# Performance work log

Hardware: AMD Instinct MI355X
Metric: run time of the kernel (lower is better)

The kernel has to match this reference:

```python
import jax, jax.numpy as jnp
import numpy as np

B, S, D, H = 2, 2048, 1024, 16
HD = D // H  # 64

def setup_inputs() -> dict:
    key = jax.random.key(0)
    k1, k2, k3 = jax.random.split(key, 3)
    x = jax.random.normal(k1, (B, S, D), dtype=jnp.float32)
    w_qkv = jax.random.normal(k2, (D, 3 * D), dtype=jnp.float32) * 0.02
    w_out = jax.random.normal(k3, (D, D), dtype=jnp.float32) * 0.02
    b_out = jnp.zeros((D,), dtype=jnp.float32)
    return {"x": x, "w_qkv": w_qkv, "w_out": w_out, "b_out": b_out}

def reference(x, w_qkv, w_out, b_out):
    # fused qkv projection (no bias)
    qkv = jnp.einsum('bsd,de->bse', x, w_qkv)            # [B,S,3D]
    q, k, v = jnp.split(qkv, 3, axis=-1)                 # each [B,S,D]
    def split_heads(t):
        return t.reshape(B, S, H, HD).transpose(0, 2, 1, 3)  # [B,H,S,HD]
    q, k, v = split_heads(q), split_heads(k), split_heads(v)
    scores = jnp.einsum('bhqd,bhkd->bhqk', q, k) / jnp.sqrt(jnp.float32(HD))
    probs = jax.nn.softmax(scores, axis=-1)              # [B,H,S,S]
    attn = jnp.einsum('bhqk,bhkd->bhqd', probs, v)       # [B,H,S,HD]
    attn = attn.transpose(0, 2, 1, 3).reshape(B, S, D)   # [B,S,D]
    out = jnp.einsum('bsd,de->bse', attn, w_out) + b_out
    return out
```

## Files before the change

### kernel.cpp

```cpp
#include <hip/hip_runtime.h>
#include <stdint.h>

#define B_  2
#define S_  2048
#define D_  1024
#define H_  16
#define HD_ 64
#define KVT 128
#define NT  (S_ / KVT)

typedef __attribute__((ext_vector_type(8))) short short8;
typedef __attribute__((ext_vector_type(4))) float f32x4;

__device__ inline unsigned short f2bf(float f) {
  union { float f; unsigned int i; } u; u.f = f;
  unsigned int r = u.i + 0x7FFFu + ((u.i >> 16) & 1u);
  return (unsigned short)(r >> 16);
}

__device__ inline uint32_t cvtpk_bf16(float lo, float hi) {
  uint32_t r;
  asm("v_cvt_pk_bf16_f32 %0, %1, %2" : "=v"(r) : "v"(lo), "v"(hi));
  return r;
}

__device__ inline float fexp2(float x) {
  float r;
  asm("v_exp_f32 %0, %1" : "=v"(r) : "v"(x));
  return r;
}

__device__ inline void gload16(const void* g, void* l) {
  __builtin_amdgcn_global_load_lds(
      (const __attribute__((address_space(1))) void*)g,
      (__attribute__((address_space(3))) void*)l,
      16, 0, 0);
}

__global__ __launch_bounds__(256)
void prologue_kernel(const float* __restrict__ x, unsigned short* __restrict__ xb,
                     const float* __restrict__ w_qkv, unsigned short* __restrict__ wqkvT,
                     const float* __restrict__ w_out, unsigned short* __restrict__ woutT) {
  __shared__ float tile[32][33];
  const int bid = blockIdx.x;
  const int t = threadIdx.x;

  if (bid < 4096) {
    int i = (bid * 256 + t) * 4;
    float4 v = *(const float4*)(x + i);
    union { unsigned short s[4]; uint2 v; } o;
    o.s[0] = f2bf(v.x); o.s[1] = f2bf(v.y); o.s[2] = f2bf(v.z); o.s[3] = f2bf(v.w);
    *(uint2*)(xb + i) = o.v;
    return;
  }

  const float* in;
  unsigned short* out;
  int R, C, bx, by;
  if (bid < 4096 + 3072) {
    int tid = bid - 4096;
    in = w_qkv; out = wqkvT; R = 1024; C = 3072;
    bx = tid % 96; by = tid / 96;
  } else {
    int tid = bid - 7168;
    in = w_out; out = woutT; R = 1024; C = 1024;
    bx = tid & 31; by = tid >> 5;
  }
  const int tx = t & 31, ty = t >> 5;
#pragma unroll
  for (int i = 0; i < 4; ++i)
    tile[ty + i * 8][tx] = in[(size_t)(by * 32 + ty + i * 8) * C + bx * 32 + tx];
  __syncthreads();
#pragma unroll
  for (int i = 0; i < 4; ++i)
    out[(size_t)(bx * 32 + ty + i * 8) * R + by * 32 + tx] = f2bf(tile[tx][ty + i * 8]);
}

__global__ __launch_bounds__(256, 3)
void gemm_qkv(const unsigned short* __restrict__ A,
              const unsigned short* __restrict__ Bt,
              unsigned short* __restrict__ qw,
              unsigned short* __restrict__ kw,
              unsigned short* __restrict__ vTw) {
  const int K = 1024;
  __shared__ __align__(16) unsigned short As[128 * 64];
  __shared__ __align__(16) unsigned short Bs[128 * 64];
  const int t  = threadIdx.x;
  const int w  = t >> 6, l = t & 63;
  const int lr = l & 15, lg = l >> 4;
  const int wr = w >> 1, wc = w & 1;
  const int bn = blockIdx.x, bm = blockIdx.y;

  const int srow = t >> 3;
  const int scol = 8 * ((t & 7) ^ (srow & 7));

  const unsigned short* Ab = A  + (size_t)(bm * 128 + srow) * K + scol;
  const unsigned short* Bb = Bt + (size_t)(bn * 128 + srow) * K + scol;

  f32x4 acc[4][4];
#pragma unroll
  for (int m = 0; m < 4; ++m)
#pragma unroll
    for (int n = 0; n < 4; ++n)
      acc[m][n] = (f32x4){0.f, 0.f, 0.f, 0.f};

  for (int kt = 0; kt < K; kt += 64) {
#pragma unroll
    for (int i = 0; i < 4; ++i) {
      gload16(Ab + (size_t)i * 32 * K + kt, &As[(size_t)(i * 256 + t) * 8]);
      gload16(Bb + (size_t)i * 32 * K + kt, &Bs[(size_t)(i * 256 + t) * 8]);
    }
    __syncthreads();
#pragma unroll
    for (int ks = 0; ks < 2; ++ks) {
      short8 af[4], bf[4];
#pragma unroll
      for (int m = 0; m < 4; ++m) {
        int row = wr * 64 + m * 16 + lr;
        af[m] = *(const short8*)&As[row * 64 + ((ks * 32 + lg * 8) ^ ((row & 7) * 8))];
      }
#pragma unroll
      for (int n = 0; n < 4; ++n) {
        int row = wc * 64 + n * 16 + lr;
        bf[n] = *(const short8*)&Bs[row * 64 + ((ks * 32 + lg * 8) ^ ((row & 7) * 8))];
      }
#pragma unroll
      for (int m = 0; m < 4; ++m)
#pragma unroll
        for (int n = 0; n < 4; ++n)
          acc[m][n] = __builtin_amdgcn_mfma_f32_16x16x32_bf16(af[m], bf[n], acc[m][n], 0, 0, 0);
    }
    __syncthreads();
  }

#pragma unroll
  for (int m = 0; m < 4; ++m)
#pragma unroll
    for (int n = 0; n < 4; ++n)
#pragma unroll
      for (int r = 0; r < 4; ++r) {
        float v = acc[m][n][r];
        int i = bm * 128 + wr * 64 + m * 16 + lg * 4 + r;
        int j = bn * 128 + wc * 64 + n * 16 + lr;
        int b = i >> 11, s = i & 2047;
        int part = j >> 10, rem = j & 1023, h = rem >> 6, hd = rem & 63;
        size_t bh = (size_t)(b * H_ + h);
        if (part == 0) {
          qw[(bh * S_ + s) * HD_ + hd] = f2bf(v * 0.1803368801f);
        } else if (part == 1) {
          kw[(bh * S_ + s) * HD_ + hd] = f2bf(v);
        } else {
          int s6 = s & 63;
          int sp = (s & ~63) | (s6 & 32) | (((s6 >> 2) & 3) << 3)
                 | (((s6 >> 4) & 1) << 2) | (s6 & 3);
          vTw[(bh * HD_ + hd) * S_ + sp] = f2bf(v);
        }
      }
}

__global__ __launch_bounds__(256)
void gemm_out(const unsigned short* __restrict__ A,
              const unsigned short* __restrict__ Bt,
              float* __restrict__ out,
              const float* __restrict__ bias) {
  const int K = 1024;
  __shared__ __align__(16) unsigned short As[128 * 64];
  __shared__ __align__(16) unsigned short Bs[64 * 64];
  const int t  = threadIdx.x;
  const int w  = t >> 6, l = t & 63;
  const int lr = l & 15, lg = l >> 4;
  const int wr = w >> 1, wc = w & 1;
  const int bn = blockIdx.x, bm = blockIdx.y;

  const int srow = t >> 3;
  const int scol = 8 * ((t & 7) ^ (srow & 7));

  const unsigned short* Ab = A  + (size_t)(bm * 128 + srow) * K + scol;
  const unsigned short* Bb = Bt + (size_t)(bn * 64 + srow) * K + scol;

  f32x4 acc[4][2];
#pragma unroll
  for (int m = 0; m < 4; ++m)
#pragma unroll
    for (int n = 0; n < 2; ++n)
      acc[m][n] = (f32x4){0.f, 0.f, 0.f, 0.f};

  for (int kt = 0; kt < K; kt += 64) {
#pragma unroll
    for (int i = 0; i < 4; ++i)
      gload16(Ab + (size_t)i * 32 * K + kt, &As[(size_t)(i * 256 + t) * 8]);
#pragma unroll
    for (int i = 0; i < 2; ++i)
      gload16(Bb + (size_t)i * 32 * K + kt, &Bs[(size_t)(i * 256 + t) * 8]);
    __syncthreads();
#pragma unroll
    for (int ks = 0; ks < 2; ++ks) {
      short8 af[4], bf[2];
#pragma unroll
      for (int m = 0; m < 4; ++m) {
        int row = wr * 64 + m * 16 + lr;
        af[m] = *(const short8*)&As[row * 64 + ((ks * 32 + lg * 8) ^ ((row & 7) * 8))];
      }
#pragma unroll
      for (int n = 0; n < 2; ++n) {
        int row = wc * 32 + n * 16 + lr;
        bf[n] = *(const short8*)&Bs[row * 64 + ((ks * 32 + lg * 8) ^ ((row & 7) * 8))];
      }
#pragma unroll
      for (int m = 0; m < 4; ++m)
#pragma unroll
        for (int n = 0; n < 2; ++n)
          acc[m][n] = __builtin_amdgcn_mfma_f32_16x16x32_bf16(af[m], bf[n], acc[m][n], 0, 0, 0);
    }
    __syncthreads();
  }

#pragma unroll
  for (int m = 0; m < 4; ++m)
#pragma unroll
    for (int n = 0; n < 2; ++n)
#pragma unroll
      for (int r = 0; r < 4; ++r) {
        int i = bm * 128 + wr * 64 + m * 16 + lg * 4 + r;
        int j = bn * 64 + wc * 32 + n * 16 + lr;
        out[(size_t)i * D_ + j] = acc[m][n][r] + bias[j];
      }
}

__global__ __launch_bounds__(256, 2)
void attn_kernel(const unsigned short* __restrict__ qw,
                 const unsigned short* __restrict__ kw,
                 const unsigned short* __restrict__ vTw,
                 unsigned short* __restrict__ attn) {
  __shared__ __align__(16) unsigned short Ks[2][KVT * 64];
  __shared__ __align__(16) unsigned short Vs[2][64 * KVT];

  const int t  = threadIdx.x;
  const int w  = t >> 6, l = t & 63;
  const int lr = l & 15, lg = l >> 4;

  const int bid = blockIdx.x;
  const int bh = (bid & 7) * 4 + ((bid >> 3) & 3);
  const int qt = bid >> 5;

  const int q0 = qt * 128 + w * 32;
  const unsigned short* Qb = qw  + (size_t)bh * S_ * HD_;
  const unsigned short* Kb = kw  + (size_t)bh * S_ * HD_;
  const unsigned short* Vb = vTw + (size_t)bh * HD_ * S_;

  const int krow = t >> 3, kcol = 8 * ((t & 7) ^ ((t >> 3) & 7));
  const int vrow = t >> 4, vcol = 8 * ((t & 15) ^ ((t >> 4) & 7));

  const short8 ones = {16256, 16256, 16256, 16256, 16256, 16256, 16256, 16256};
  const f32x4 FZERO = (f32x4){0.f, 0.f, 0.f, 0.f};

  short8 qf[2][2];
#pragma unroll
  for (int m = 0; m < 2; ++m)
#pragma unroll
    for (int ks = 0; ks < 2; ++ks)
      qf[m][ks] = *(const short8*)&Qb[(size_t)(q0 + m * 16 + lr) * HD_ + ks * 32 + lg * 8];

  f32x4 of[2][4];
  f32x4 osum[2];
#pragma unroll
  for (int m = 0; m < 2; ++m) {
#pragma unroll
    for (int n = 0; n < 4; ++n) of[m][n] = FZERO;
    osum[m] = FZERO;
  }

#pragma unroll
  for (int i = 0; i < 4; ++i) {
    gload16(Kb + (size_t)(i * 32 + krow) * HD_ + kcol, &Ks[0][(i * 256 + t) * 8]);
    gload16(Vb + (size_t)(i * 16 + vrow) * S_ + vcol,  &Vs[0][(i * 256 + t) * 8]);
  }
  __syncthreads();

  int cur = 0;
  for (int tt = 0; tt < NT; ++tt) {
    if (tt + 1 < NT) {
      const int kt = (tt + 1) * KVT;
#pragma unroll
      for (int i = 0; i < 4; ++i) {
        gload16(Kb + (size_t)(kt + i * 32 + krow) * HD_ + kcol, &Ks[cur ^ 1][(i * 256 + t) * 8]);
        gload16(Vb + (size_t)(i * 16 + vrow) * S_ + kt + vcol,  &Vs[cur ^ 1][(i * 256 + t) * 8]);
      }
    }

    f32x4 sfT[2][8];
    __builtin_amdgcn_s_setprio(1);
#pragma unroll
    for (int n = 0; n < 8; ++n) {
      int row = n * 16 + lr;
      short8 kf0 = *(const short8*)&Ks[cur][row * 64 + ((lg * 8) ^ ((row & 7) * 8))];
      sfT[0][n] = __builtin_amdgcn_mfma_f32_16x16x32_bf16(kf0, qf[0][0], FZERO, 0, 0, 0);
      sfT[1][n] = __builtin_amdgcn_mfma_f32_16x16x32_bf16(kf0, qf[1][0], FZERO, 0, 0, 0);
      short8 kf1 = *(const short8*)&Ks[cur][row * 64 + ((32 + lg * 8) ^ ((row & 7) * 8))];
      sfT[0][n] = __builtin_amdgcn_mfma_f32_16x16x32_bf16(kf1, qf[0][1], sfT[0][n], 0, 0, 0);
      sfT[1][n] = __builtin_amdgcn_mfma_f32_16x16x32_bf16(kf1, qf[1][1], sfT[1][n], 0, 0, 0);
    }
    __builtin_amdgcn_s_setprio(0);

    union { uint32_t u[4]; short8 v; } pb[2][4];
#pragma unroll
    for (int m = 0; m < 2; ++m) {
#pragma unroll
      for (int n = 0; n < 8; ++n) {
        sfT[m][n][0] = fexp2(sfT[m][n][0]);
        sfT[m][n][1] = fexp2(sfT[m][n][1]);
        sfT[m][n][2] = fexp2(sfT[m][n][2]);
        sfT[m][n][3] = fexp2(sfT[m][n][3]);
      }
#pragma unroll
      for (int kk = 0; kk < 4; ++kk) {
        pb[m][kk].u[0] = cvtpk_bf16(sfT[m][2 * kk][0],     sfT[m][2 * kk][1]);
        pb[m][kk].u[1] = cvtpk_bf16(sfT[m][2 * kk][2],     sfT[m][2 * kk][3]);
        pb[m][kk].u[2] = cvtpk_bf16(sfT[m][2 * kk + 1][0], sfT[m][2 * kk + 1][1]);
        pb[m][kk].u[3] = cvtpk_bf16(sfT[m][2 * kk + 1][2], sfT[m][2 * kk + 1][3]);
      }
    }

    __builtin_amdgcn_s_setprio(1);
#pragma unroll
    for (int nd = 0; nd < 4; ++nd)
#pragma unroll
      for (int kk = 0; kk < 4; ++kk) {
        int row = nd * 16 + lr;
        short8 vf = *(const short8*)&Vs[cur][row * 128 + ((kk * 32 + lg * 8) ^ ((row & 7) * 8))];
        of[0][nd] = __builtin_amdgcn_mfma_f32_16x16x32_bf16(vf, pb[0][kk].v, of[0][nd], 0, 0, 0);
        of[1][nd] = __builtin_amdgcn_mfma_f32_16x16x32_bf16(vf, pb[1][kk].v, of[1][nd], 0, 0, 0);
      }
#pragma unroll
    for (int m = 0; m < 2; ++m)
#pragma unroll
      for (int kk = 0; kk < 4; ++kk)
        osum[m] = __builtin_amdgcn_mfma_f32_16x16x32_bf16(ones, pb[m][kk].v, osum[m], 0, 0, 0);
    __builtin_amdgcn_s_setprio(0);

    __syncthreads();
    cur ^= 1;
  }

  const int b = bh >> 4, h = bh & 15;
#pragma unroll
  for (int m = 0; m < 2; ++m) {
    float inv = 1.0f / osum[m][0];
    int q = q0 + m * 16 + lr;
#pragma unroll
    for (int nd = 0; nd < 4; ++nd)
#pragma unroll
      for (int r = 0; r < 4; ++r)
        attn[((size_t)b * S_ + q) * D_ + h * 64 + nd * 16 + lg * 4 + r] =
            f2bf(of[m][nd][r] * inv);
  }
}

extern "C" void kernel_launch(void* const* d_in, const int* in_sizes, int n_in,
                              void* d_out, int out_size, void* d_ws, size_t ws_size,
                              hipStream_t stream) {
  const float* x     = (const float*)d_in[0];
  const float* w_qkv = (const float*)d_in[1];
  const float* w_out = (const float*)d_in[2];
  const float* b_out = (const float*)d_in[3];
  float* out = (float*)d_out;

  char* p = (char*)d_ws;
  unsigned short* xb    = (unsigned short*)p; p += (size_t)4096 * 1024 * 2;
  unsigned short* wqkvT = (unsigned short*)p; p += (size_t)3072 * 1024 * 2;
  unsigned short* woutT = (unsigned short*)p; p += (size_t)1024 * 1024 * 2;
  unsigned short* qws   = (unsigned short*)p; p += (size_t)B_ * H_ * S_ * HD_ * 2;
  unsigned short* kws   = (unsigned short*)p; p += (size_t)B_ * H_ * S_ * HD_ * 2;
  unsigned short* vTws  = (unsigned short*)p; p += (size_t)B_ * H_ * S_ * HD_ * 2;
  unsigned short* attnb = (unsigned short*)p; p += (size_t)4096 * 1024 * 2;

  prologue_kernel<<<8192, 256, 0, stream>>>(x, xb, w_qkv, wqkvT, w_out, woutT);

  gemm_qkv<<<dim3(24, 32), 256, 0, stream>>>(xb, wqkvT, qws, kws, vTws);

  attn_kernel<<<512, 256, 0, stream>>>(qws, kws, vTws, attnb);

  gemm_out<<<dim3(16, 32), 256, 0, stream>>>(attnb, woutT, out, b_out);
}
```

Measured before the change: 102.6 us.

## Split attention KV range in two with partial outputs and a combine kernel

Splits each attention block's KV sequence into two halves, so twice as many blocks run (1024 instead of 512), each over 1024 keys with a 64-wide KV tile and a higher occupancy hint. Each half writes unnormalized bf16 partial outputs and row sums to workspace. A new combine kernel adds the halves, normalizes, and writes the head-interleaved attention output. This aims to fill the CUs better, at the cost of an extra launch, extra global traffic, and an added bf16 rounding of the partials.

```diff
diff --git a/kernel.cpp b/kernel.cpp
--- a/kernel.cpp
+++ b/kernel.cpp
@@ -6,8 +6,8 @@
 #define D_  1024
 #define H_  16
 #define HD_ 64
-#define KVT 128
-#define NT  (S_ / KVT)
+#define KVT 64
+#define NTT 16
 
 typedef __attribute__((ext_vector_type(8))) short short8;
 typedef __attribute__((ext_vector_type(4))) float f32x4;
@@ -16,6 +16,10 @@
   union { float f; unsigned int i; } u; u.f = f;
   unsigned int r = u.i + 0x7FFFu + ((u.i >> 16) & 1u);
   return (unsigned short)(r >> 16);
+}
+
+__device__ inline float bf2f(unsigned short u) {
+  union { unsigned int i; float f; } x; x.i = ((unsigned int)u) << 16; return x.f;
 }
 
 __device__ inline uint32_t cvtpk_bf16(float lo, float hi) {
@@ -227,11 +231,12 @@
       }
 }
 
-__global__ __launch_bounds__(256, 2)
+__global__ __launch_bounds__(256, 4)
 void attn_kernel(const unsigned short* __restrict__ qw,
                  const unsigned short* __restrict__ kw,
                  const unsigned short* __restrict__ vTw,
-                 unsigned short* __restrict__ attn) {
+                 unsigned short* __restrict__ part,
+                 float* __restrict__ sums) {
   __shared__ __align__(16) unsigned short Ks[2][KVT * 64];
   __shared__ __align__(16) unsigned short Vs[2][64 * KVT];
 
@@ -240,16 +245,17 @@
   const int lr = l & 15, lg = l >> 4;
 
   const int bid = blockIdx.x;
-  const int bh = (bid & 7) * 4 + ((bid >> 3) & 3);
-  const int qt = bid >> 5;
+  const int bh   = (bid & 7) * 4 + ((bid >> 3) & 3);
+  const int rest = bid >> 5;
+  const int qt   = rest >> 1;
+  const int half = rest & 1;
 
   const int q0 = qt * 128 + w * 32;
   const unsigned short* Qb = qw  + (size_t)bh * S_ * HD_;
-  const unsigned short* Kb = kw  + (size_t)bh * S_ * HD_;
-  const unsigned short* Vb = vTw + (size_t)bh * HD_ * S_;
+  const unsigned short* Kb = kw  + (size_t)bh * S_ * HD_ + (size_t)half * 1024 * HD_;
+  const unsigned short* Vb = vTw + (size_t)bh * HD_ * S_ + half * 1024;
 
   const int krow = t >> 3, kcol = 8 * ((t & 7) ^ ((t >> 3) & 7));
-  const int vrow = t >> 4, vcol = 8 * ((t & 15) ^ ((t >> 4) & 7));
 
   const short8 ones = {16256, 16256, 16256, 16256, 16256, 16256, 16256, 16256};
   const f32x4 FZERO = (f32x4){0.f, 0.f, 0.f, 0.f};
@@ -271,27 +277,29 @@
   }
 
 #pragma unroll
-  for (int i = 0; i < 4; ++i) {
-    gload16(Kb + (size_t)(i * 32 + krow) * HD_ + kcol, &Ks[0][(i * 256 + t) * 8]);
-    gload16(Vb + (size_t)(i * 16 + vrow) * S_ + vcol,  &Vs[0][(i * 256 + t) * 8]);
+  for (int i = 0; i < 2; ++i) {
+    int row = i * 32 + krow;
+    gload16(Kb + (size_t)row * HD_ + kcol, &Ks[0][(i * 256 + t) * 8]);
+    gload16(Vb + (size_t)row * S_ + kcol,  &Vs[0][(i * 256 + t) * 8]);
   }
   __syncthreads();
 
   int cur = 0;
-  for (int tt = 0; tt < NT; ++tt) {
-    if (tt + 1 < NT) {
+  for (int tt = 0; tt < NTT; ++tt) {
+    if (tt + 1 < NTT) {
       const int kt = (tt + 1) * KVT;
 #pragma unroll
-      for (int i = 0; i < 4; ++i) {
-        gload16(Kb + (size_t)(kt + i * 32 + krow) * HD_ + kcol, &Ks[cur ^ 1][(i * 256 + t) * 8]);
-        gload16(Vb + (size_t)(i * 16 + vrow) * S_ + kt + vcol,  &Vs[cur ^ 1][(i * 256 + t) * 8]);
-      }
-    }
-
-    f32x4 sfT[2][8];
+      for (int i = 0; i < 2; ++i) {
+        int row = i * 32 + krow;
+        gload16(Kb + (size_t)(kt + row) * HD_ + kcol, &Ks[cur ^ 1][(i * 256 + t) * 8]);
+        gload16(Vb + (size_t)row * S_ + kt + kcol,    &Vs[cur ^ 1][(i * 256 + t) * 8]);
+      }
+    }
+
+    f32x4 sfT[2][4];
     __builtin_amdgcn_s_setprio(1);
 #pragma unroll
-    for (int n = 0; n < 8; ++n) {
+    for (int n = 0; n < 4; ++n) {
       int row = n * 16 + lr;
       short8 kf0 = *(const short8*)&Ks[cur][row * 64 + ((lg * 8) ^ ((row & 7) * 8))];
       sfT[0][n] = __builtin_amdgcn_mfma_f32_16x16x32_bf16(kf0, qf[0][0], FZERO, 0, 0, 0);
@@ -302,18 +310,18 @@
     }
     __builtin_amdgcn_s_setprio(0);
 
-    union { uint32_t u[4]; short8 v; } pb[2][4];
+    union { uint32_t u[4]; short8 v; } pb[2][2];
 #pragma unroll
     for (int m = 0; m < 2; ++m) {
 #pragma unroll
-      for (int n = 0; n < 8; ++n) {
+      for (int n = 0; n < 4; ++n) {
         sfT[m][n][0] = fexp2(sfT[m][n][0]);
         sfT[m][n][1] = fexp2(sfT[m][n][1]);
         sfT[m][n][2] = fexp2(sfT[m][n][2]);
         sfT[m][n][3] = fexp2(sfT[m][n][3]);
       }
 #pragma unroll
-      for (int kk = 0; kk < 4; ++kk) {
+      for (int kk = 0; kk < 2; ++kk) {
         pb[m][kk].u[0] = cvtpk_bf16(sfT[m][2 * kk][0],     sfT[m][2 * kk][1]);
         pb[m][kk].u[1] = cvtpk_bf16(sfT[m][2 * kk][2],     sfT[m][2 * kk][3]);
         pb[m][kk].u[2] = cvtpk_bf16(sfT[m][2 * kk + 1][0], sfT[m][2 * kk + 1][1]);
@@ -325,16 +333,16 @@
 #pragma unroll
     for (int nd = 0; nd < 4; ++nd)
 #pragma unroll
-      for (int kk = 0; kk < 4; ++kk) {
+      for (int kk = 0; kk < 2; ++kk) {
         int row = nd * 16 + lr;
-        short8 vf = *(const short8*)&Vs[cur][row * 128 + ((kk * 32 + lg * 8) ^ ((row & 7) * 8))];
+        short8 vf = *(const short8*)&Vs[cur][row * 64 + ((kk * 32 + lg * 8) ^ ((row & 7) * 8))];
         of[0][nd] = __builtin_amdgcn_mfma_f32_16x16x32_bf16(vf, pb[0][kk].v, of[0][nd], 0, 0, 0);
         of[1][nd] = __builtin_amdgcn_mfma_f32_16x16x32_bf16(vf, pb[1][kk].v, of[1][nd], 0, 0, 0);
       }
 #pragma unroll
     for (int m = 0; m < 2; ++m)
 #pragma unroll
-      for (int kk = 0; kk < 4; ++kk)
+      for (int kk = 0; kk < 2; ++kk)
         osum[m] = __builtin_amdgcn_mfma_f32_16x16x32_bf16(ones, pb[m][kk].v, osum[m], 0, 0, 0);
     __builtin_amdgcn_s_setprio(0);
 
@@ -342,18 +350,44 @@
     cur ^= 1;
   }
 
-  const int b = bh >> 4, h = bh & 15;
+  unsigned short* Pw = part + (size_t)half * (32 * 2048 * 64);
+  float* Sw = sums + (size_t)half * (32 * 2048);
 #pragma unroll
   for (int m = 0; m < 2; ++m) {
-    float inv = 1.0f / osum[m][0];
     int q = q0 + m * 16 + lr;
-#pragma unroll
-    for (int nd = 0; nd < 4; ++nd)
-#pragma unroll
-      for (int r = 0; r < 4; ++r)
-        attn[((size_t)b * S_ + q) * D_ + h * 64 + nd * 16 + lg * 4 + r] =
-            f2bf(of[m][nd][r] * inv);
-  }
+    size_t row64 = (size_t)(bh * 2048 + q) * 64;
+    if (lg == 0) Sw[bh * 2048 + q] = osum[m][0];
+#pragma unroll
+    for (int nd = 0; nd < 4; ++nd) {
+      union { unsigned short s_[4]; uint2 v; } o;
+      o.s_[0] = f2bf(of[m][nd][0]);
+      o.s_[1] = f2bf(of[m][nd][1]);
+      o.s_[2] = f2bf(of[m][nd][2]);
+      o.s_[3] = f2bf(of[m][nd][3]);
+      *(uint2*)&Pw[row64 + nd * 16 + lg * 4] = o.v;
+    }
+  }
+}
+
+__global__ __launch_bounds__(256)
+void combine_kernel(const unsigned short* __restrict__ part,
+                    const float* __restrict__ sums,
+                    unsigned short* __restrict__ attnb) {
+  const int bb = blockIdx.x;
+  const int bh = bb >> 6, qc = bb & 63;
+  const int t = threadIdx.x;
+  const int ql = t >> 3, dv = t & 7;
+  const int q = qc * 32 + ql;
+  const size_t row = (size_t)(bh * 2048 + q);
+  const float inv = 1.0f / (sums[row] + sums[32 * 2048 + row]);
+  const short8 a = *(const short8*)&part[row * 64 + dv * 8];
+  const short8 b = *(const short8*)&part[(size_t)(32 * 2048 * 64) + row * 64 + dv * 8];
+  union { unsigned short s_[8]; uint4 v; } o;
+#pragma unroll
+  for (int r = 0; r < 8; ++r)
+    o.s_[r] = f2bf((bf2f((unsigned short)a[r]) + bf2f((unsigned short)b[r])) * inv);
+  const int bq = bh >> 4, h = bh & 15;
+  *(uint4*)&attnb[((size_t)(bq * 2048 + q)) * D_ + h * 64 + dv * 8] = o.v;
 }
 
 extern "C" void kernel_launch(void* const* d_in, const int* in_sizes, int n_in,
@@ -373,12 +407,15 @@
   unsigned short* kws   = (unsigned short*)p; p += (size_t)B_ * H_ * S_ * HD_ * 2;
   unsigned short* vTws  = (unsigned short*)p; p += (size_t)B_ * H_ * S_ * HD_ * 2;
   unsigned short* attnb = (unsigned short*)p; p += (size_t)4096 * 1024 * 2;
+  unsigned short* partw = (unsigned short*)p; p += (size_t)2 * 32 * 2048 * 64 * 2;
+  float*          sumsw = (float*)p;          p += (size_t)2 * 32 * 2048 * 4;
 
   prologue_kernel<<<8192, 256, 0, stream>>>(x, xb, w_qkv, wqkvT, w_out, woutT);
 
   gemm_qkv<<<dim3(24, 32), 256, 0, stream>>>(xb, wqkvT, qws, kws, vTws);
 
-  attn_kernel<<<512, 256, 0, stream>>>(qws, kws, vTws, attnb);
+  attn_kernel<<<1024, 256, 0, stream>>>(qws, kws, vTws, partw, sumsw);
+  combine_kernel<<<2048, 256, 0, stream>>>(partw, sumsw, attnb);
 
   gemm_out<<<dim3(16, 32), 256, 0, stream>>>(attnb, woutT, out, b_out);
 }
```

Result: slower. 109.1 us (+6.4%).
